# Optimization experiments

Measured on AMD Instinct MI355X. Metric: run time of the kernel, lower is better.

Reference implementation:

```python
import jax, jax.numpy as jnp
import numpy as np

LN_EPS = 1e-5
NEG_SLOPE = 0.01  # torch LeakyReLU default
H, D = 16, 64


def _layernorm(x, g, b):
    m = jnp.mean(x, axis=-1, keepdims=True)
    v = jnp.var(x, axis=-1, keepdims=True)
    return (x - m) * jax.lax.rsqrt(v + LN_EPS) * g + b


def _mlp(x, ln_g, ln_b, W1, b1, W2, b2):
    h = _layernorm(x, ln_g, ln_b)
    h = jax.nn.gelu(h @ W1 + b1, approximate=False)
    return h @ W2 + b2


def _gather_nodes(node_msg, edge_index):
    # node_msg: (b,n,c), edge_index: (b,n,k) -> (b,n,k,c)
    return jax.vmap(lambda nm, ei: nm[ei])(node_msg, edge_index)


def setup_inputs() -> dict:
    key = jax.random.key(0)
    ks = jax.random.split(key, 16)
    b, n, k = 2, 1024, 32
    dim, pdim, msg_dim = 512, 256, 256
    s = 0.02
    inp = {
        'node_repr': jax.random.normal(ks[0], (b, n, dim), jnp.float32),
        'edge_repr': jax.random.normal(ks[1], (b, n, k, pdim), jnp.float32),
        'edge_index': jax.random.randint(ks[2], (b, n, k), 0, n, jnp.int32),
        'edge_mask': jax.random.randint(ks[3], (b, n, k), 0, 2, jnp.int32),
        'mask_bw': jnp.ones((b, n, k, 1), jnp.float32),
        'W_edge_msg': s * jax.random.normal(ks[4], (pdim, msg_dim), jnp.float32),
        'W_node_src': s * jax.random.normal(ks[5], (dim, msg_dim), jnp.float32),
        'W_node_tgt': s * jax.random.normal(ks[6], (dim, msg_dim), jnp.float32),
        'msg_ln_g': jnp.ones((msg_dim,), jnp.float32),
        'msg_ln_b': jnp.zeros((msg_dim,), jnp.float32),
        'msg_W1': s * jax.random.normal(ks[7], (msg_dim, 4 * msg_dim), jnp.float32),
        'msg_b1': jnp.zeros((4 * msg_dim,), jnp.float32),
        'msg_W2': s * jax.random.normal(ks[8], (4 * msg_dim, msg_dim), jnp.float32),
        'msg_b2': jnp.zeros((msg_dim,), jnp.float32),
        'W_gate': jnp.zeros((dim, msg_dim), jnp.float32),   # init_weights: zeros
        'b_gate': -jnp.ones((msg_dim,), jnp.float32),       # init_weights: -1
        'W_out': s * jax.random.normal(ks[9], (msg_dim, dim), jnp.float32),
        'W_msg': s * jax.random.normal(ks[10], (msg_dim, msg_dim), jnp.float32),
        'W_attn_bias': s * jax.random.normal(ks[11], (msg_dim, H), jnp.float32),
        'W_gat_value': s * jax.random.normal(ks[12], (msg_dim, H * D), jnp.float32),
        'W_gat_gate': jnp.zeros((dim, H * D), jnp.float32),
        'b_gat_gate': -jnp.ones((H * D,), jnp.float32),
        'W_gat_out': s * jax.random.normal(ks[13], (H * D, dim), jnp.float32),
        'node_ln_g': jnp.ones((dim,), jnp.float32),
        'node_ln_b': jnp.zeros((dim,), jnp.float32),
        'node_W1': s * jax.random.normal(ks[14], (dim, 4 * dim), jnp.float32),
        'node_b1': jnp.zeros((4 * dim,), jnp.float32),
        'node_W2': s * jax.random.normal(ks[15], (4 * dim, dim), jnp.float32),
        'node_b2': jnp.zeros((dim,), jnp.float32),
    }
    return inp


def reference(node_repr, edge_repr, edge_index, edge_mask, mask_bw,
              W_edge_msg, W_node_src, W_node_tgt,
              msg_ln_g, msg_ln_b, msg_W1, msg_b1, msg_W2, msg_b2,
              W_gate, b_gate, W_out,
              W_msg, W_attn_bias, W_gat_value, W_gat_gate, b_gat_gate, W_gat_out,
              node_ln_g, node_ln_b, node_W1, node_b1, node_W2, node_b2):
    b, n, k = edge_index.shape
    em_bool = edge_mask.astype(bool)          # (b,n,k)
    em_f = edge_mask.astype(node_repr.dtype)

    # edge-wise message: edge proj + gathered src node proj + broadcast tgt node proj
    node_msg = node_repr @ W_node_src                      # (b,n,msg)
    msg = edge_repr @ W_edge_msg \
        + _gather_nodes(node_msg, edge_index) * mask_bw \
        + (node_repr @ W_node_tgt)[:, :, None, :]          # (b,n,k,msg)
    msg = _mlp(msg, msg_ln_g, msg_ln_b, msg_W1, msg_b1, msg_W2, msg_b2)
    msg = jnp.where(em_bool[..., None], msg, 0.0)

    # global (mean-pooled, gated) path
    o = (msg * em_f[..., None]).sum(-2) / (em_f.sum(-1, keepdims=True) + 1e-6)
    o = jax.nn.sigmoid(node_repr @ W_gate + b_gate) * o
    dh = o @ W_out                                         # (b,n,dim)

    # GAT path: per-node attention over its k neighbors
    ab = jnp.where(NEG_SLOPE < 1, jax.nn.leaky_relu(msg @ W_msg, NEG_SLOPE), msg) @ W_attn_bias  # (b,n,k,H)
    ab = jnp.where(em_bool[..., None], ab, -jnp.finfo(ab.dtype).max)
    attn = jax.nn.softmax(ab, axis=2)                      # softmax over k
    v = (msg @ W_gat_value).reshape(b, n, k, H, D)
    og = jnp.einsum('bnkh,bnkhd->bnhd', attn, v).reshape(b, n, H * D)
    og = jax.nn.sigmoid(node_repr @ W_gat_gate + b_gat_gate) * og
    dh = dh + og @ W_gat_out

    # residual + node MLP (dropout is identity in eval mode)
    node_repr = node_repr + dh
    node_repr = node_repr + _mlp(node_repr, node_ln_g, node_ln_b, node_W1, node_b1, node_W2, node_b2)
    return node_repr
```

## Files before the change

kernel.cpp:

```cpp
#include <hip/hip_runtime.h>
#include <hip/hip_bf16.h>

typedef unsigned short u16;
typedef short s16x8 __attribute__((ext_vector_type(8)));
typedef float f32x4 __attribute__((ext_vector_type(4)));
typedef float f32x8 __attribute__((ext_vector_type(8)));
typedef u16 u16x8 __attribute__((ext_vector_type(8)));

#define DEV static __device__ __forceinline__

DEV float b2f(u16 u){ unsigned int i=((unsigned int)u)<<16; float f; __builtin_memcpy(&f,&i,4); return f; }
DEV u16 f2b(float x){ __hip_bfloat16 h=__float2bfloat16(x); u16 u; __builtin_memcpy(&u,&h,2); return u; }
DEV f32x4 MFMA(s16x8 a, s16x8 b, f32x4 c){ return __builtin_amdgcn_mfma_f32_16x16x32_bf16(a,b,c,0,0,0); }
DEV s16x8 LD8(const u16* p){ return *(const s16x8*)p; }
DEV float gelu_fast(float x){
  return x / (1.f + __expf(-1.702f*x));
}
DEV float sigmf(float x){ return 1.0f/(1.0f+__expf(-x)); }

DEV void gload16(const u16* g, u16* l){
  __builtin_amdgcn_global_load_lds((const __attribute__((address_space(1))) void*)g,
                                   (__attribute__((address_space(3))) void*)l, 16, 0, 0);
}

#define WS_WeT   0
#define WS_W1T   65536
#define WS_W2T   327680
#define WS_WmT   589824
#define WS_WvT   655360
#define WS_WoT   917504
#define WS_WgoT  1048576
#define WS_nW1T  1572864
#define WS_nW2T  2621440
#define WS_SrcT  3670016
#define WS_TgtT  3801088
#define WS_GateT 3932160
#define WS_GgT   4063232
#define WS_NM    4587520
#define WS_TGT   5111808
#define WS_GP    5636096
#define WS_GG    6160384
#define WS_MSG   8257536
#define WS_U2    8257536
#define WS_X     10354688
#define WS_Y     12451840
#define WS_WM    25034752
#define WS_U1    33423360
#define WS_YE    33947648
#define WS_H     50724864

struct P13 { const float* p[13]; };
__device__ const int TR_START[14] = {0,16,80,144,160,224,256,384,640,896,928,960,992,1120};
__device__ const int TR_R[13]   = {256,256,1024,256,256,256,1024,512,2048,512,512,512,512};
__device__ const int TR_C[13]   = {256,1024,256,256,1024,512,512,2048,512,256,256,256,1024};
__device__ const int TR_DST[13] = {WS_WeT,WS_W1T,WS_W2T,WS_WmT,WS_WvT,WS_WoT,WS_WgoT,
                                   WS_nW1T,WS_nW2T,WS_SrcT,WS_TgtT,WS_GateT,WS_GgT};

__global__ __launch_bounds__(256) void k_transpose(P13 ps, u16* __restrict__ ws){
  __shared__ alignas(16) u16 Ts[64][72];
  const int t = threadIdx.x;
  int bid = blockIdx.x;
  int mi = 0;
  #pragma unroll 1
  while (bid >= TR_START[mi+1]) ++mi;
  const float* src = ps.p[mi];
  const int R = TR_R[mi], C = TR_C[mi];
  u16* dst = ws + TR_DST[mi];
  const int ti = bid - TR_START[mi];
  const int tcn = C >> 6;
  const int tr = ti / tcn, tc = ti % tcn;
  {
    const int row = t >> 2, cs = (t & 3) * 16;
    const float* sp = src + (tr*64 + row)*C + tc*64 + cs;
    u16x8 a, b;
    #pragma unroll
    for (int i=0;i<8;i++){ a[i]=f2b(sp[i]); b[i]=f2b(sp[8+i]); }
    *(u16x8*)&Ts[row][cs]   = a;
    *(u16x8*)&Ts[row][cs+8] = b;
  }
  __syncthreads();
  {
    const int col = t >> 2, rs = (t & 3) * 16;
    u16x8 a, b;
    #pragma unroll
    for (int i=0;i<8;i++){ a[i]=Ts[rs+i][col]; b[i]=Ts[rs+8+i][col]; }
    u16* dp = dst + (tc*64 + col)*R + tr*64 + rs;
    *(u16x8*)dp = a;
    *(u16x8*)(dp+8) = b;
  }
}

__global__ __launch_bounds__(256) void k_cvtnode(const float* __restrict__ src, u16* __restrict__ dst){
  const int i = (blockIdx.x*256 + threadIdx.x)*8;
  f32x8 v = *(const f32x8*)(src + i);
  u16x8 o;
  #pragma unroll
  for (int j=0;j<8;j++) o[j] = f2b(v[j]);
  *(u16x8*)(dst + i) = o;
}

__global__ __launch_bounds__(256) void k_proj(const float* __restrict__ bgate,
                                              const float* __restrict__ bgg,
                                              u16* __restrict__ ws){
  const int t=threadIdx.x, lid=t&63, w=t>>6, g=lid>>4, q=lid&15;
  const int rb = blockIdx.x, yb = blockIdx.y;
  const u16* nb = ws + WS_H;
  const u16* BT; u16* dst; int Nseg, colbase, act=0; const float* bias=nullptr;
  if (yb < 4){ BT=ws+WS_SrcT;  dst=ws+WS_NM; Nseg=256;  colbase=yb*64; }
  else if (yb < 8){ BT=ws+WS_TgtT;  dst=ws+WS_TGT; Nseg=256; colbase=(yb-4)*64; }
  else if (yb < 12){ BT=ws+WS_GateT; dst=ws+WS_GP; Nseg=256; colbase=(yb-8)*64; act=1; bias=bgate; }
  else { BT=ws+WS_GgT; dst=ws+WS_GG; Nseg=1024; colbase=(yb-12)*64; act=1; bias=bgg; }
  const int wr=(w>>1)*32, wcl=(w&1)*32;
  f32x4 acc[2][2] = {};
  for (int kk=0; kk<512; kk+=32){
    s16x8 af[2], bfr[2];
    #pragma unroll
    for (int i=0;i<2;i++) af[i] = LD8(nb + (rb*64 + wr + i*16 + q)*512 + kk + 8*g);
    #pragma unroll
    for (int j=0;j<2;j++) bfr[j] = LD8(BT + (colbase + wcl + j*16 + q)*512 + kk + 8*g);
    #pragma unroll
    for (int i=0;i<2;i++)
      #pragma unroll
      for (int j=0;j<2;j++) acc[i][j] = MFMA(af[i], bfr[j], acc[i][j]);
  }
  #pragma unroll
  for (int i=0;i<2;i++)
    #pragma unroll
    for (int j=0;j<2;j++)
      #pragma unroll
      for (int r=0;r<4;r++){
        const int row = rb*64 + wr + i*16 + g*4 + r;
        const int col = wcl + j*16 + q;
        float v = acc[i][j][r];
        if (act) v = sigmf(v + bias[colbase+col]);
        dst[row*Nseg + colbase + col] = f2b(v);
      }
}

#define GB_S 528
__global__ __launch_bounds__(512) void k_edgepre(
    const float* __restrict__ edge_repr, const int* __restrict__ edge_index,
    const float* __restrict__ mask_bw,
    const float* __restrict__ ln_g, const float* __restrict__ ln_b,
    u16* __restrict__ ws)
{
  __shared__ alignas(16) char SH[64*GB_S];
  __shared__ float rsS[4][64], rsQ[4][64];
  __shared__ int idxL[64]; __shared__ float mbwL[64];

  const int t=threadIdx.x, lid=t&63, w=t>>6, g=lid>>4, q=lid&15;
  const int R0 = blockIdx.x * 64;
  const int wrg = (w>>2)*32;
  const int wcl = (w&3)*64;
  u16* As = (u16*)SH;
  u16* Bs = (u16*)(SH + 4096);

  if (t < 64){
    idxL[t] = edge_index[R0+t];
    mbwL[t] = mask_bw[R0+t];
  }
  __syncthreads();

  const u16* nm = ws + WS_NM;
  const u16* tg = ws + WS_TGT;
  #pragma unroll
  for (int it=0; it<4; ++it){
    const int v = t + 512*it;
    const int row = v >> 5;
    const int sc  = (v & 31) * 8;
    const int er  = R0 + row;
    const int gnd = er >> 5;
    const int bi  = gnd >> 10;
    const int srow = bi*1024 + idxL[row];
    const float mb = mbwL[row];
    u16x8 nv = *(const u16x8*)(nm + srow*256 + sc);
    u16x8 tv = *(const u16x8*)(tg + gnd*256 + sc);
    u16x8 ov;
    #pragma unroll
    for (int j2=0;j2<8;j2++) ov[j2] = f2b(b2f(nv[j2])*mb + b2f(tv[j2]));
    *(u16x8*)(SH + row*GB_S + 2*sc) = ov;
  }
  __syncthreads();
  f32x4 acc[2][4];
  #pragma unroll
  for (int i=0;i<2;i++)
    #pragma unroll
    for (int r=0;r<4;r++){
      const int row = wrg + i*16 + g*4 + r;
      #pragma unroll
      for (int j=0;j<4;j++){
        const int col = wcl + j*16 + q;
        acc[i][j][r] = b2f(*(const u16*)(SH + row*GB_S + 2*col));
      }
    }
  for (int kk=0; kk<256; kk+=32){
    __syncthreads();
    if (t < 256){
      const int row = t >> 2, c0 = (t & 3) * 8;
      const float* sp = edge_repr + (R0 + row)*256 + kk + c0;
      f32x8 fv = *(const f32x8*)sp;
      u16x8 av;
      #pragma unroll
      for (int j2=0;j2<8;j2++) av[j2] = f2b(fv[j2]);
      *(u16x8*)(As + row*32 + c0) = av;
    }
    #pragma unroll
    for (int j=0;j<2;j++){
      const int s = t + 512*j;
      const int brow = s >> 2, ko = (s & 3) * 8;
      u16* ldsB = Bs + (512*j + w*64)*8;
      gload16(ws + WS_WeT + brow*256 + kk + ko, ldsB);
    }
    __syncthreads();
    s16x8 af[2], bfr[4];
    #pragma unroll
    for (int i=0;i<2;i++) af[i]  = *(const s16x8*)(As + (wrg + i*16 + q)*32 + g*8);
    #pragma unroll
    for (int j=0;j<4;j++) bfr[j] = *(const s16x8*)(Bs + (wcl + j*16 + q)*32 + g*8);
    #pragma unroll
    for (int i=0;i<2;i++)
      #pragma unroll
      for (int j=0;j<4;j++) acc[i][j] = MFMA(af[i], bfr[j], acc[i][j]);
  }
  #pragma unroll
  for (int i=0;i<2;i++)
    #pragma unroll
    for (int r=0;r<4;r++){
      float s=0.f, s2=0.f;
      #pragma unroll
      for (int j=0;j<4;j++){ float v=acc[i][j][r]; s+=v; s2+=v*v; }
      #pragma unroll
      for (int m=1;m<16;m<<=1){ s += __shfl_xor(s,m,64); s2 += __shfl_xor(s2,m,64); }
      if (q==0){ const int row=wrg+i*16+g*4+r; rsS[w&3][row]=s; rsQ[w&3][row]=s2; }
    }
  __syncthreads();
  #pragma unroll
  for (int i=0;i<2;i++)
    #pragma unroll
    for (int r=0;r<4;r++){
      const int row = wrg + i*16 + g*4 + r;
      const float s  = rsS[0][row]+rsS[1][row]+rsS[2][row]+rsS[3][row];
      const float s2 = rsQ[0][row]+rsQ[1][row]+rsQ[2][row]+rsQ[3][row];
      const float mean = s*(1.f/256.f);
      const float var  = s2*(1.f/256.f) - mean*mean;
      const float rstd = rsqrtf(var + 1e-5f);
      #pragma unroll
      for (int j=0;j<4;j++){
        const int col = wcl + j*16 + q;
        *(u16*)(SH + row*GB_S + 2*col) = f2b((acc[i][j][r]-mean)*rstd*ln_g[col] + ln_b[col]);
      }
    }
  __syncthreads();
  u16* Ye = ws + WS_YE;
  #pragma unroll
  for (int it=0; it<4; ++it){
    const int v = t + 512*it;
    const int row = v >> 5, sc = (v & 31)*8;
    *(u16x8*)(Ye + (R0+row)*256 + sc) = *(const u16x8*)(SH + row*GB_S + 2*sc);
  }
}

__global__ __launch_bounds__(256) void k_mlp1(const u16* __restrict__ A,
                                              const u16* __restrict__ BT,
                                              const float* __restrict__ b1,
                                              u16* __restrict__ H){
  __shared__ alignas(16) u16 SH2[64*136];
  u16* As = SH2;
  u16* Bs = SH2 + 4096;
  const int t=threadIdx.x, lid=t&63, w=t>>6, g=lid>>4, q=lid&15;
  const int r0 = blockIdx.x*128, n0 = blockIdx.y*128;
  const int wc3 = w*32;
  f32x4 acc[8][2] = {};
  for (int kk=0;kk<256;kk+=32){
    __syncthreads();
    #pragma unroll
    for (int j=0;j<2;j++){
      const int v = t + 256*j;
      const int row = v>>2, sg = (v&3)*8;
      gload16(A  + (r0+row)*256 + kk + sg, As + (w*64 + 256*j)*8);
      gload16(BT + (n0+row)*256 + kk + sg, Bs + (w*64 + 256*j)*8);
    }
    __syncthreads();
    s16x8 bf_[2];
    #pragma unroll
    for (int j=0;j<2;j++) bf_[j] = *(const s16x8*)(Bs + (wc3 + j*16 + q)*32 + g*8);
    #pragma unroll
    for (int i=0;i<8;i++){
      s16x8 af = *(const s16x8*)(As + (i*16+q)*32 + g*8);
      #pragma unroll
      for (int j=0;j<2;j++) acc[i][j] = MFMA(af, bf_[j], acc[i][j]);
    }
  }
  #pragma unroll
  for (int p=0;p<2;p++){
    __syncthreads();
    #pragma unroll
    for (int i2=0;i2<4;i2++)
      #pragma unroll
      for (int j=0;j<2;j++)
        #pragma unroll
        for (int r=0;r<4;r++){
          const int rl = i2*16 + g*4 + r;
          const int cl = wc3 + j*16 + q;
          SH2[rl*136 + cl] = f2b(gelu_fast(acc[p*4+i2][j][r] + b1[n0 + cl]));
        }
    __syncthreads();
    #pragma unroll
    for (int it=0; it<4; ++it){
      const int v = t + 256*it;
      const int rrow = v >> 4, sc = (v & 15)*8;
      *(u16x8*)(H + (r0 + p*64 + rrow)*1024 + n0 + sc) = *(const u16x8*)(SH2 + rrow*136 + sc);
    }
  }
}

__global__ __launch_bounds__(256) void k_mlp2(const u16* __restrict__ A,
                                              const u16* __restrict__ BT,
                                              const float* __restrict__ b2,
                                              const int* __restrict__ em,
                                              u16* __restrict__ msg){
  __shared__ alignas(16) u16 As[128*32];
  __shared__ alignas(16) u16 Bs[128*32];
  __shared__ int emL[128];
  const int t=threadIdx.x, lid=t&63, w=t>>6, g=lid>>4, q=lid&15;
  const int r0 = blockIdx.x*128, n0 = blockIdx.y*128;
  const int wr=(w>>1)*64, wc2=(w&1)*64;
  if (t < 128) emL[t] = em[r0 + t];
  f32x4 acc[4][4] = {};
  for (int kk=0;kk<1024;kk+=32){
    __syncthreads();
    #pragma unroll
    for (int j=0;j<2;j++){
      const int v = t + 256*j;
      const int row = v>>2, sg = (v&3)*8;
      gload16(A  + (r0+row)*1024 + kk + sg, As + (w*64 + 256*j)*8);
      gload16(BT + (n0+row)*1024 + kk + sg, Bs + (w*64 + 256*j)*8);
    }
    __syncthreads();
    s16x8 af[4], bf_[4];
    #pragma unroll
    for (int i=0;i<4;i++) af[i]  = *(const s16x8*)(As + (wr+i*16+q)*32 + g*8);
    #pragma unroll
    for (int j=0;j<4;j++) bf_[j] = *(const s16x8*)(Bs + (wc2+j*16+q)*32 + g*8);
    #pragma unroll
    for (int i=0;i<4;i++)
      #pragma unroll
      for (int j=0;j<4;j++) acc[i][j] = MFMA(af[i], bf_[j], acc[i][j]);
  }
  #pragma unroll
  for (int i=0;i<4;i++)
    #pragma unroll
    for (int j=0;j<4;j++)
      #pragma unroll
      for (int r=0;r<4;r++){
        const int rl  = wr + i*16 + g*4 + r;
        const int col = n0 + wc2 + j*16 + q;
        float v = acc[i][j][r] + b2[col];
        if (!emL[rl]) v = 0.f;
        msg[(r0+rl)*256 + col] = f2b(v);
      }
}

__global__ __launch_bounds__(256) void k_tm(const u16* __restrict__ A,
                                            const u16* __restrict__ BT,
                                            u16* __restrict__ Tm){
  __shared__ alignas(16) u16 SH2[64*136];
  u16* As = SH2;
  u16* Bs = SH2 + 4096;
  const int t=threadIdx.x, lid=t&63, w=t>>6, g=lid>>4, q=lid&15;
  const int r0 = blockIdx.x*128, n0 = blockIdx.y*128;
  const int wc3 = w*32;
  f32x4 acc[8][2] = {};
  for (int kk=0;kk<256;kk+=32){
    __syncthreads();
    #pragma unroll
    for (int j=0;j<2;j++){
      const int v = t + 256*j;
      const int row = v>>2, sg = (v&3)*8;
      gload16(A  + (r0+row)*256 + kk + sg, As + (w*64 + 256*j)*8);
      gload16(BT + (n0+row)*256 + kk + sg, Bs + (w*64 + 256*j)*8);
    }
    __syncthreads();
    s16x8 bf_[2];
    #pragma unroll
    for (int j=0;j<2;j++) bf_[j] = *(const s16x8*)(Bs + (wc3 + j*16 + q)*32 + g*8);
    #pragma unroll
    for (int i=0;i<8;i++){
      s16x8 af = *(const s16x8*)(As + (i*16+q)*32 + g*8);
      #pragma unroll
      for (int j=0;j<2;j++) acc[i][j] = MFMA(af, bf_[j], acc[i][j]);
    }
  }
  #pragma unroll
  for (int p=0;p<2;p++){
    __syncthreads();
    #pragma unroll
    for (int i2=0;i2<4;i2++)
      #pragma unroll
      for (int j=0;j<2;j++)
        #pragma unroll
        for (int r=0;r<4;r++){
          const int rl = i2*16 + g*4 + r;
          const int cl = wc3 + j*16 + q;
          float v = acc[p*4+i2][j][r];
          SH2[rl*136 + cl] = f2b(v > 0.f ? v : 0.01f*v);
        }
    __syncthreads();
    #pragma unroll
    for (int it=0; it<4; ++it){
      const int v = t + 256*it;
      const int rrow = v >> 4, sc = (v & 15)*8;
      *(u16x8*)(Tm + (r0 + p*64 + rrow)*256 + n0 + sc) = *(const u16x8*)(SH2 + rrow*136 + sc);
    }
  }
}

__global__ __launch_bounds__(256) void k_ab(const u16* __restrict__ A,
                                            const float* __restrict__ Wab,
                                            float* __restrict__ AB){
  __shared__ alignas(16) u16 As[128*32];
  __shared__ alignas(16) char WbT[16*528];
  const int t=threadIdx.x, lid=t&63, w=t>>6, g=lid>>4, q=lid&15;
  const int r0 = blockIdx.x*128;
  {
    const float* wr_ = Wab + t*16;
    #pragma unroll
    for (int h=0;h<16;h++) *(u16*)(WbT + h*528 + 2*t) = f2b(wr_[h]);
  }
  f32x4 acc[2] = {};
  for (int kk=0;kk<256;kk+=32){
    __syncthreads();
    #pragma unroll
    for (int j=0;j<2;j++){
      const int s = t + 256*j;
      const int row = s>>2, ko = (s&3)*8;
      gload16(A + (r0+row)*256 + kk + ko, As + (w*64 + 256*j)*8);
    }
    __syncthreads();
    s16x8 bf_ = *(const s16x8*)(WbT + q*528 + 2*(kk + 8*g));
    #pragma unroll
    for (int i=0;i<2;i++){
      s16x8 af = *(const s16x8*)(As + (w*32 + i*16 + q)*32 + g*8);
      acc[i] = MFMA(af, bf_, acc[i]);
    }
  }
  #pragma unroll
  for (int i=0;i<2;i++)
    #pragma unroll
    for (int r=0;r<4;r++){
      const int row = r0 + w*32 + i*16 + g*4 + r;
      AB[row*16 + q] = acc[i][r];
    }
}

#define AM_S 528
#define MT_S 80
__global__ __launch_bounds__(256) void k_attn2(const int* __restrict__ edge_mask,
                                               u16* __restrict__ ws){
  __shared__ alignas(16) char Am[32*AM_S];
  __shared__ alignas(16) char Mt[256*MT_S];
  __shared__ alignas(16) char Pb[16*80];
  __shared__ float Pp[32][16];
  __shared__ int emL[32];
  __shared__ float cntS;

  const int t=threadIdx.x, lid=t&63, w=t>>6, g=lid>>4, q=lid&15;
  const int nd = blockIdx.x;
  const int wc = w*64;
  const u16* msg = ws + WS_MSG + nd*32*256;
  const float* ab = (const float*)(ws + WS_YE) + nd*32*16;

  if (t < 32) emL[t] = edge_mask[nd*32 + t];
  #pragma unroll
  for (int it=0; it<4; ++it){
    const int v = t + 256*it;
    const int row = v >> 5, sc = (v & 31)*8;
    u16x8 val = *(const u16x8*)(msg + row*256 + sc);
    *(u16x8*)(Am + row*AM_S + 2*sc) = val;
  }
  {
    const int k = t >> 4, h = t & 15;
    Pp[k][h]    = ab[k*16 + h];
    Pp[k+16][h] = ab[(k+16)*16 + h];
  }
  __syncthreads();
  if (t == 0){ float c=0.f; for (int k=0;k<32;k++) c += emL[k]?1.f:0.f; cntS=c; }
  {
    const int c = t;
    #pragma unroll 1
    for (int k=0;k<32;k++){
      u16 vv = *(const u16*)(Am + k*AM_S + 2*c);
      *(u16*)(Mt + c*MT_S + 2*k) = vv;
    }
  }
  if (t < 16){
    const int h = t;
    float m = -3.4028235e38f;
    float pv[32];
    for (int k=0;k<32;k++){ pv[k] = emL[k] ? Pp[k][h] : -3.4028235e38f; m = fmaxf(m, pv[k]); }
    float s = 0.f;
    float ev[32];
    for (int k=0;k<32;k++){ ev[k]=__expf(pv[k]-m); s+=ev[k]; }
    const float inv = 1.f/s;
    for (int k=0;k<32;k++) *(u16*)(Pb + h*80 + 2*k) = f2b(ev[k]*inv);
  }
  __syncthreads();
  {
    s16x8 pa = *(const s16x8*)(Pb + q*80 + 2*(8*g));
    f32x4 wmac[4] = {};
    #pragma unroll
    for (int j=0;j<4;j++){
      s16x8 mb = *(const s16x8*)(Mt + (wc + j*16 + q)*MT_S + 2*(8*g));
      wmac[j] = MFMA(pa, mb, wmac[j]);
    }
    u16* wmw = ws + WS_WM;
    #pragma unroll
    for (int j=0;j<4;j++)
      #pragma unroll
      for (int r=0;r<4;r++){
        const int hh = g*4 + r;
        const int col = wc + j*16 + q;
        wmw[hh*(2048*256) + nd*256 + col] = f2b(wmac[j][r]);
      }
  }
  {
    const int c = t;
    float s = 0.f;
    #pragma unroll 1
    for (int k=0;k<32;k++) s += b2f(*(const u16*)(Am + k*AM_S + 2*c));
    const float o = s / (cntS + 1e-6f);
    ws[WS_U1 + nd*256 + c] = f2b(o * b2f(ws[WS_GP + nd*256 + c]));
  }
}

__global__ __launch_bounds__(256) void k_og(u16* __restrict__ ws){
  const int t=threadIdx.x, lid=t&63, w=t>>6, g=lid>>4, q=lid&15;
  const int rb=blockIdx.x, h=blockIdx.y;
  const int wr=(w>>1)*32, wcl=(w&1)*32;
  const u16* A  = ws + WS_WM  + h*(2048*256);
  const u16* BT = ws + WS_WvT;
  f32x4 acc[2][2] = {};
  for (int kk=0;kk<256;kk+=32){
    s16x8 af[2], bfr[2];
    #pragma unroll
    for (int i=0;i<2;i++) af[i] = LD8(A + (rb*64 + wr + i*16 + q)*256 + kk + 8*g);
    #pragma unroll
    for (int j=0;j<2;j++) bfr[j] = LD8(BT + (h*64 + wcl + j*16 + q)*256 + kk + 8*g);
    #pragma unroll
    for (int i=0;i<2;i++)
      #pragma unroll
      for (int j=0;j<2;j++) acc[i][j] = MFMA(af[i], bfr[j], acc[i][j]);
  }
  #pragma unroll
  for (int i=0;i<2;i++)
    #pragma unroll
    for (int j=0;j<2;j++)
      #pragma unroll
      for (int r=0;r<4;r++){
        const int row = rb*64 + wr + i*16 + g*4 + r;
        const int col = h*64 + wcl + j*16 + q;
        const float gv = b2f(ws[WS_GG + row*1024 + col]);
        ws[WS_U2 + row*1024 + col] = f2b(acc[i][j][r] * gv);
      }
}

__global__ __launch_bounds__(256) void k_dh(const float* __restrict__ node_repr, u16* __restrict__ ws){
  const int t=threadIdx.x, lid=t&63, w=t>>6, g=lid>>4, q=lid&15;
  const int rb=blockIdx.x, cb=blockIdx.y*64;
  const int wr=(w>>1)*32, wcl=(w&1)*32;
  float* Xf = (float*)(ws + WS_X);
  f32x4 acc[2][2] = {};
  for (int kk=0;kk<256;kk+=32){
    s16x8 af[2], bfr[2];
    #pragma unroll
    for (int i=0;i<2;i++) af[i] = LD8(ws + WS_U1 + (rb*64 + wr + i*16 + q)*256 + kk + 8*g);
    #pragma unroll
    for (int j=0;j<2;j++) bfr[j] = LD8(ws + WS_WoT + (cb + wcl + j*16 + q)*256 + kk + 8*g);
    #pragma unroll
    for (int i=0;i<2;i++)
      #pragma unroll
      for (int j=0;j<2;j++) acc[i][j] = MFMA(af[i], bfr[j], acc[i][j]);
  }
  for (int kk=0;kk<1024;kk+=32){
    s16x8 af[2], bfr[2];
    #pragma unroll
    for (int i=0;i<2;i++) af[i] = LD8(ws + WS_U2 + (rb*64 + wr + i*16 + q)*1024 + kk + 8*g);
    #pragma unroll
    for (int j=0;j<2;j++) bfr[j] = LD8(ws + WS_WgoT + (cb + wcl + j*16 + q)*1024 + kk + 8*g);
    #pragma unroll
    for (int i=0;i<2;i++)
      #pragma unroll
      for (int j=0;j<2;j++) acc[i][j] = MFMA(af[i], bfr[j], acc[i][j]);
  }
  #pragma unroll
  for (int i=0;i<2;i++)
    #pragma unroll
    for (int j=0;j<2;j++)
      #pragma unroll
      for (int r=0;r<4;r++){
        const int row = rb*64 + wr + i*16 + g*4 + r;
        const int col = cb + wcl + j*16 + q;
        Xf[row*512 + col] = acc[i][j][r] + node_repr[row*512 + col];
      }
}

__global__ __launch_bounds__(256) void k_ln512(const float* __restrict__ g_, const float* __restrict__ b_,
                                               u16* __restrict__ ws){
  const int t=threadIdx.x, wid=t>>6, lane=t&63;
  const int row = blockIdx.x*4 + wid;
  const float* xr = (const float*)(ws + WS_X) + row*512;
  f32x8 xv = *(const f32x8*)(xr + lane*8);
  float s=0.f, s2=0.f;
  #pragma unroll
  for (int i=0;i<8;i++){ s+=xv[i]; s2+=xv[i]*xv[i]; }
  #pragma unroll
  for (int m=1;m<64;m<<=1){ s += __shfl_xor(s,m,64); s2 += __shfl_xor(s2,m,64); }
  const float mean = s*(1.f/512.f);
  const float var  = s2*(1.f/512.f) - mean*mean;
  const float rstd = rsqrtf(var + 1e-5f);
  u16x8 yv;
  #pragma unroll
  for (int i=0;i<8;i++) yv[i] = f2b((xv[i]-mean)*rstd*g_[lane*8+i] + b_[lane*8+i]);
  *(u16x8*)(ws + WS_Y + row*512 + lane*8) = yv;
}

__global__ __launch_bounds__(256) void k_nmlp1(const u16* __restrict__ A,
                                               const u16* __restrict__ BT,
                                               const float* __restrict__ b1,
                                               u16* __restrict__ H){
  __shared__ alignas(16) u16 SH2[64*136];
  u16* As = SH2;
  u16* Bs = SH2 + 4096;
  const int t=threadIdx.x, lid=t&63, w=t>>6, g=lid>>4, q=lid&15;
  const int r0 = blockIdx.x*128, n0 = blockIdx.y*128;
  const int wc3 = w*32;
  f32x4 acc[8][2] = {};
  for (int kk=0;kk<512;kk+=32){
    __syncthreads();
    #pragma unroll
    for (int j=0;j<2;j++){
      const int v = t + 256*j;
      const int row = v>>2, sg = (v&3)*8;
      gload16(A  + (r0+row)*512 + kk + sg, As + (w*64 + 256*j)*8);
      gload16(BT + (n0+row)*512 + kk + sg, Bs + (w*64 + 256*j)*8);
    }
    __syncthreads();
    s16x8 bf_[2];
    #pragma unroll
    for (int j=0;j<2;j++) bf_[j] = *(const s16x8*)(Bs + (wc3 + j*16 + q)*32 + g*8);
    #pragma unroll
    for (int i=0;i<8;i++){
      s16x8 af = *(const s16x8*)(As + (i*16+q)*32 + g*8);
      #pragma unroll
      for (int j=0;j<2;j++) acc[i][j] = MFMA(af, bf_[j], acc[i][j]);
    }
  }
  #pragma unroll
  for (int p=0;p<2;p++){
    __syncthreads();
    #pragma unroll
    for (int i2=0;i2<4;i2++)
      #pragma unroll
      for (int j=0;j<2;j++)
        #pragma unroll
        for (int r=0;r<4;r++){
          const int rl = i2*16 + g*4 + r;
          const int cl = wc3 + j*16 + q;
          SH2[rl*136 + cl] = f2b(gelu_fast(acc[p*4+i2][j][r] + b1[n0 + cl]));
        }
    __syncthreads();
    #pragma unroll
    for (int it=0; it<4; ++it){
      const int v = t + 256*it;
      const int rrow = v >> 4, sc = (v & 15)*8;
      *(u16x8*)(H + (r0 + p*64 + rrow)*2048 + n0 + sc) = *(const u16x8*)(SH2 + rrow*136 + sc);
    }
  }
}

__global__ __launch_bounds__(256) void k_nmlp2(const u16* __restrict__ A,
                                               const u16* __restrict__ BT,
                                               const float* __restrict__ b2,
                                               const float* __restrict__ Xf,
                                               float* __restrict__ out){
  __shared__ alignas(16) u16 As[64*32];
  __shared__ alignas(16) u16 Bs[64*32];
  const int t=threadIdx.x, lid=t&63, w=t>>6, g=lid>>4, q=lid&15;
  const int r0 = blockIdx.x*64, n0 = blockIdx.y*64;
  const int wr=(w>>1)*32, wc2=(w&1)*32;
  f32x4 acc[2][2] = {};
  for (int kk=0;kk<2048;kk+=32){
    __syncthreads();
    {
      const int row = t>>2, sg = (t&3)*8;
      gload16(A  + (r0+row)*2048 + kk + sg, As + (w*64)*8);
      gload16(BT + (n0+row)*2048 + kk + sg, Bs + (w*64)*8);
    }
    __syncthreads();
    s16x8 af[2], bf_[2];
    #pragma unroll
    for (int i=0;i<2;i++) af[i]  = *(const s16x8*)(As + (wr+i*16+q)*32 + g*8);
    #pragma unroll
    for (int j=0;j<2;j++) bf_[j] = *(const s16x8*)(Bs + (wc2+j*16+q)*32 + g*8);
    #pragma unroll
    for (int i=0;i<2;i++)
      #pragma unroll
      for (int j=0;j<2;j++) acc[i][j] = MFMA(af[i], bf_[j], acc[i][j]);
  }
  #pragma unroll
  for (int i=0;i<2;i++)
    #pragma unroll
    for (int j=0;j<2;j++)
      #pragma unroll
      for (int r=0;r<4;r++){
        const int row = r0 + wr + i*16 + g*4 + r;
        const int col = n0 + wc2 + j*16 + q;
        out[row*512 + col] = acc[i][j][r] + b2[col] + Xf[row*512 + col];
      }
}

extern "C" void kernel_launch(void* const* d_in, const int* in_sizes, int n_in,
                              void* d_out, int out_size, void* d_ws, size_t ws_size,
                              hipStream_t stream){
  (void)in_sizes; (void)n_in; (void)out_size; (void)ws_size;
  const float* node_repr = (const float*)d_in[0];
  const float* edge_repr = (const float*)d_in[1];
  const int* edge_index = (const int*)d_in[2];
  const int* edge_mask  = (const int*)d_in[3];
  const float* mask_bw = (const float*)d_in[4];
  u16* ws = (u16*)d_ws;

  P13 ps;
  const int srcIdx[13] = {5,10,12,17,19,16,22,25,27,6,7,14,20};
  for (int i=0;i<13;i++) ps.p[i] = (const float*)d_in[srcIdx[i]];

  hipLaunchKernelGGL(k_transpose, dim3(1120), dim3(256), 0, stream, ps, ws);
  hipLaunchKernelGGL(k_cvtnode, dim3(512), dim3(256), 0, stream, node_repr, ws + WS_H);
  hipLaunchKernelGGL(k_proj, dim3(32,28), dim3(256), 0, stream,
                     (const float*)d_in[15], (const float*)d_in[21], ws);
  hipLaunchKernelGGL(k_edgepre, dim3(1024), dim3(512), 0, stream,
                     edge_repr, edge_index, mask_bw,
                     (const float*)d_in[8], (const float*)d_in[9], ws);
  for (int grp=0; grp<2; ++grp){
    const u16* Ag = ws + WS_YE + grp*32768*256;
    u16* Hg = ws + WS_H;
    u16* msgg = ws + WS_MSG + grp*32768*256;
    const int* emg = edge_mask + grp*32768;
    hipLaunchKernelGGL(k_mlp1, dim3(256,8), dim3(256), 0, stream,
                       Ag, ws + WS_W1T, (const float*)d_in[11], Hg);
    hipLaunchKernelGGL(k_mlp2, dim3(256,2), dim3(256), 0, stream,
                       Hg, ws + WS_W2T, (const float*)d_in[13], emg, msgg);
  }
  hipLaunchKernelGGL(k_tm, dim3(512,2), dim3(256), 0, stream,
                     ws + WS_MSG, ws + WS_WmT, ws + WS_H);
  hipLaunchKernelGGL(k_ab, dim3(512), dim3(256), 0, stream,
                     ws + WS_H, (const float*)d_in[18], (float*)(ws + WS_YE));
  hipLaunchKernelGGL(k_attn2, dim3(2048), dim3(256), 0, stream,
                     edge_mask, ws);
  hipLaunchKernelGGL(k_og, dim3(32,16), dim3(256), 0, stream, ws);
  hipLaunchKernelGGL(k_dh, dim3(32,8), dim3(256), 0, stream, node_repr, ws);
  hipLaunchKernelGGL(k_ln512, dim3(512), dim3(256), 0, stream,
                     (const float*)d_in[23], (const float*)d_in[24], ws);
  hipLaunchKernelGGL(k_nmlp1, dim3(16,16), dim3(256), 0, stream,
                     ws + WS_Y, ws + WS_nW1T, (const float*)d_in[26], ws + WS_H);
  hipLaunchKernelGGL(k_nmlp2, dim3(32,8), dim3(256), 0, stream,
                     ws + WS_H, ws + WS_nW2T, (const float*)d_in[28],
                     (const float*)(ws + WS_X), (float*)d_out);
}
```

Before: 352.6 us.

## Double-buffer LDS tiles in MLP1, Tm and node-MLP1 GEMM kernels

Converts the K loops of three bf16 MFMA GEMM kernels from a load-barrier-compute pattern to a two-stage LDS ping-pong. The next K-slice is loaded asynchronously with global_load_lds while MFMAs run on the current slice, and one barrier per iteration replaces two. The goal is to hide global-load latency behind matrix math. In exchange, LDS per block roughly doubles, which may reduce occupancy, and an unused vrow/vsg pair is left in the code.

```diff
diff --git a/kernel.cpp b/kernel.cpp
--- a/kernel.cpp
+++ b/kernel.cpp
@@ -264,23 +264,36 @@
                                               const u16* __restrict__ BT,
                                               const float* __restrict__ b1,
                                               u16* __restrict__ H){
-  __shared__ alignas(16) u16 SH2[64*136];
-  u16* As = SH2;
-  u16* Bs = SH2 + 4096;
+  __shared__ alignas(16) u16 SH2[16384];
   const int t=threadIdx.x, lid=t&63, w=t>>6, g=lid>>4, q=lid&15;
   const int r0 = blockIdx.x*128, n0 = blockIdx.y*128;
   const int wc3 = w*32;
+  const int vrow = (t + 0) >> 2;
+  const int vsg  = (t & 3) * 8;
   f32x4 acc[8][2] = {};
-  for (int kk=0;kk<256;kk+=32){
-    __syncthreads();
-    #pragma unroll
-    for (int j=0;j<2;j++){
-      const int v = t + 256*j;
-      const int row = v>>2, sg = (v&3)*8;
-      gload16(A  + (r0+row)*256 + kk + sg, As + (w*64 + 256*j)*8);
-      gload16(BT + (n0+row)*256 + kk + sg, Bs + (w*64 + 256*j)*8);
-    }
-    __syncthreads();
+  #pragma unroll
+  for (int j=0;j<2;j++){
+    const int v = t + 256*j;
+    const int row = v>>2, sg = (v&3)*8;
+    gload16(A  + (r0+row)*256 + sg,        SH2 + (w*64 + 256*j)*8);
+    gload16(BT + (n0+row)*256 + sg,        SH2 + 4096 + (w*64 + 256*j)*8);
+  }
+  __syncthreads();
+  for (int ks=0; ks<8; ++ks){
+    const int cur = ks & 1;
+    if (ks < 7){
+      const int kk = (ks+1)*32;
+      const int nb = cur ^ 1;
+      #pragma unroll
+      for (int j=0;j<2;j++){
+        const int v = t + 256*j;
+        const int row = v>>2, sg = (v&3)*8;
+        gload16(A  + (r0+row)*256 + kk + sg, SH2 + nb*8192 + (w*64 + 256*j)*8);
+        gload16(BT + (n0+row)*256 + kk + sg, SH2 + nb*8192 + 4096 + (w*64 + 256*j)*8);
+      }
+    }
+    const u16* As = SH2 + cur*8192;
+    const u16* Bs = As + 4096;
     s16x8 bf_[2];
     #pragma unroll
     for (int j=0;j<2;j++) bf_[j] = *(const s16x8*)(Bs + (wc3 + j*16 + q)*32 + g*8);
@@ -290,7 +303,9 @@
       #pragma unroll
       for (int j=0;j<2;j++) acc[i][j] = MFMA(af, bf_[j], acc[i][j]);
     }
-  }
+    __syncthreads();
+  }
+  (void)vrow; (void)vsg;
   #pragma unroll
   for (int p=0;p<2;p++){
     __syncthreads();
@@ -364,23 +379,34 @@
 __global__ __launch_bounds__(256) void k_tm(const u16* __restrict__ A,
                                             const u16* __restrict__ BT,
                                             u16* __restrict__ Tm){
-  __shared__ alignas(16) u16 SH2[64*136];
-  u16* As = SH2;
-  u16* Bs = SH2 + 4096;
+  __shared__ alignas(16) u16 SH2[16384];
   const int t=threadIdx.x, lid=t&63, w=t>>6, g=lid>>4, q=lid&15;
   const int r0 = blockIdx.x*128, n0 = blockIdx.y*128;
   const int wc3 = w*32;
   f32x4 acc[8][2] = {};
-  for (int kk=0;kk<256;kk+=32){
-    __syncthreads();
-    #pragma unroll
-    for (int j=0;j<2;j++){
-      const int v = t + 256*j;
-      const int row = v>>2, sg = (v&3)*8;
-      gload16(A  + (r0+row)*256 + kk + sg, As + (w*64 + 256*j)*8);
-      gload16(BT + (n0+row)*256 + kk + sg, Bs + (w*64 + 256*j)*8);
-    }
-    __syncthreads();
+  #pragma unroll
+  for (int j=0;j<2;j++){
+    const int v = t + 256*j;
+    const int row = v>>2, sg = (v&3)*8;
+    gload16(A  + (r0+row)*256 + sg, SH2 + (w*64 + 256*j)*8);
+    gload16(BT + (n0+row)*256 + sg, SH2 + 4096 + (w*64 + 256*j)*8);
+  }
+  __syncthreads();
+  for (int ks=0; ks<8; ++ks){
+    const int cur = ks & 1;
+    if (ks < 7){
+      const int kk = (ks+1)*32;
+      const int nb = cur ^ 1;
+      #pragma unroll
+      for (int j=0;j<2;j++){
+        const int v = t + 256*j;
+        const int row = v>>2, sg = (v&3)*8;
+        gload16(A  + (r0+row)*256 + kk + sg, SH2 + nb*8192 + (w*64 + 256*j)*8);
+        gload16(BT + (n0+row)*256 + kk + sg, SH2 + nb*8192 + 4096 + (w*64 + 256*j)*8);
+      }
+    }
+    const u16* As = SH2 + cur*8192;
+    const u16* Bs = As + 4096;
     s16x8 bf_[2];
     #pragma unroll
     for (int j=0;j<2;j++) bf_[j] = *(const s16x8*)(Bs + (wc3 + j*16 + q)*32 + g*8);
@@ -390,6 +416,7 @@
       #pragma unroll
       for (int j=0;j<2;j++) acc[i][j] = MFMA(af, bf_[j], acc[i][j]);
     }
+    __syncthreads();
   }
   #pragma unroll
   for (int p=0;p<2;p++){
@@ -628,23 +655,34 @@
                                                const u16* __restrict__ BT,
                                                const float* __restrict__ b1,
                                                u16* __restrict__ H){
-  __shared__ alignas(16) u16 SH2[64*136];
-  u16* As = SH2;
-  u16* Bs = SH2 + 4096;
+  __shared__ alignas(16) u16 SH2[16384];
   const int t=threadIdx.x, lid=t&63, w=t>>6, g=lid>>4, q=lid&15;
   const int r0 = blockIdx.x*128, n0 = blockIdx.y*128;
   const int wc3 = w*32;
   f32x4 acc[8][2] = {};
-  for (int kk=0;kk<512;kk+=32){
-    __syncthreads();
-    #pragma unroll
-    for (int j=0;j<2;j++){
-      const int v = t + 256*j;
-      const int row = v>>2, sg = (v&3)*8;
-      gload16(A  + (r0+row)*512 + kk + sg, As + (w*64 + 256*j)*8);
-      gload16(BT + (n0+row)*512 + kk + sg, Bs + (w*64 + 256*j)*8);
-    }
-    __syncthreads();
+  #pragma unroll
+  for (int j=0;j<2;j++){
+    const int v = t + 256*j;
+    const int row = v>>2, sg = (v&3)*8;
+    gload16(A  + (r0+row)*512 + sg, SH2 + (w*64 + 256*j)*8);
+    gload16(BT + (n0+row)*512 + sg, SH2 + 4096 + (w*64 + 256*j)*8);
+  }
+  __syncthreads();
+  for (int ks=0; ks<16; ++ks){
+    const int cur = ks & 1;
+    if (ks < 15){
+      const int kk = (ks+1)*32;
+      const int nb = cur ^ 1;
+      #pragma unroll
+      for (int j=0;j<2;j++){
+        const int v = t + 256*j;
+        const int row = v>>2, sg = (v&3)*8;
+        gload16(A  + (r0+row)*512 + kk + sg, SH2 + nb*8192 + (w*64 + 256*j)*8);
+        gload16(BT + (n0+row)*512 + kk + sg, SH2 + nb*8192 + 4096 + (w*64 + 256*j)*8);
+      }
+    }
+    const u16* As = SH2 + cur*8192;
+    const u16* Bs = As + 4096;
     s16x8 bf_[2];
     #pragma unroll
     for (int j=0;j<2;j++) bf_[j] = *(const s16x8*)(Bs + (wc3 + j*16 + q)*32 + g*8);
@@ -654,6 +692,7 @@
       #pragma unroll
       for (int j=0;j<2;j++) acc[i][j] = MFMA(af, bf_[j], acc[i][j]);
     }
+    __syncthreads();
   }
   #pragma unroll
   for (int p=0;p<2;p++){
```

After: 345.9 us. Within noise of the previous version (-1.9%).
